# Kernel optimization log

Measured on AMD Instinct MI355X. Metric: run time of the kernel, lower is better.

## Reference

```python
import jax, jax.numpy as jnp
import numpy as np

D = 1024
BATCH = 32768
QJL_DIM = 1024

# Optimal 3-bit (8-level) Lloyd-Max quantizer for the standard normal N(0,1).
# Rotated coordinates of Gaussian inputs are ~N(0,1) since Pi is orthogonal.
_CENTROIDS = np.array([-2.1520, -1.3439, -0.7560, -0.2451,
                        0.2451,  0.7560,  1.3439,  2.1520], dtype=np.float32)
_BOUNDARIES = np.array([-1.7480, -1.0500, -0.5006, 0.0,
                         0.5006,  1.0500,  1.7480], dtype=np.float32)


def setup_inputs() -> dict:
    key = jax.random.key(0)
    kx, kpi, ks = jax.random.split(key, 3)
    x = jax.random.normal(kx, (BATCH, D), dtype=jnp.float32)
    # Haar rotation: orthogonal matrix via QR of a Gaussian matrix
    G = jax.random.normal(kpi, (D, D), dtype=jnp.float32)
    Pi, _ = jnp.linalg.qr(G)
    # QJL projection matrix: iid N(0,1), shape (m, d)
    S = jax.random.normal(ks, (QJL_DIM, D), dtype=jnp.float32)
    return {
        "x": x,
        "Pi": Pi,
        "S": S,
        "centroids": jnp.asarray(_CENTROIDS),
        "boundaries": jnp.asarray(_BOUNDARIES),
    }


def reference(x, Pi, S, centroids, boundaries):
    # --- Stage 1: MSE quantizer (rotate -> Lloyd-Max -> unrotate) ---
    y = x @ Pi.T                                  # (B, d) rotated coordinates
    idx = jnp.searchsorted(boundaries, y)         # (B, d) int32 in [0, 8)
    y_hat = centroids[idx]                        # (B, d) per-coordinate dequant
    x_hat = y_hat @ Pi                            # unrotate back to original frame

    # --- Stage 2: QJL on the residual ---
    residual = x - x_hat                          # (B, d)
    residual_norm = jnp.linalg.norm(residual, axis=-1)   # (B,)
    projected = residual @ S.T                    # (B, m)
    # torch.sign with sign(0) forced to +1
    qjl_signs = jnp.where(projected >= 0, 1.0, -1.0).astype(x.dtype)

    return (idx, qjl_signs, residual_norm)
```

## Files before the change

### kernel.cpp

```cpp
#include <hip/hip_runtime.h>

#define DK 1024
#define NB 32768
#define BM 128
#define BN 128
#define BKT 16

#define MASK_MAIN 0x0000000080000000ull

template<int MODE>
__global__ __launch_bounds__(256)
void gk(const float* __restrict__ A,
        const float* __restrict__ W,
        const float* __restrict__ X,
        const float* __restrict__ cent,
        const float* __restrict__ bnd,
        float* __restrict__ out)
{
    __shared__ float As[BKT][BM];
    __shared__ float Bs[BKT][BN];
    __shared__ float centS[8];

    const int tid = threadIdx.x;
    const int tx8 = tid & 15, ty8 = tid >> 4;
    const int m0 = blockIdx.y * BM;
    const int n0 = blockIdx.x * BN;

    const int arow = tid >> 1;
    const int ak0  = (tid & 1) * 8;
    const int brow = tid >> 4;
    const int bn0  = (tid & 15) * 8;

    if (MODE == 1 && tid < 8) centS[tid] = cent[tid];

    float chn[8][8], tot[8][8];
#pragma unroll
    for (int i = 0; i < 8; ++i)
#pragma unroll
        for (int j = 0; j < 8; ++j) { chn[i][j] = 0.0f; tot[i][j] = 0.0f; }

    for (int kt = 0; kt < DK / BKT; ++kt) {
        const int k0 = kt * BKT;
        __syncthreads();

        {
            const float4 v0 = *(const float4*)&A[(size_t)(m0 + arow) * DK + k0 + ak0];
            const float4 v1 = *(const float4*)&A[(size_t)(m0 + arow) * DK + k0 + ak0 + 4];
            if (MODE == 1) {
                As[ak0 + 0][arow] = centS[(int)v0.x];
                As[ak0 + 1][arow] = centS[(int)v0.y];
                As[ak0 + 2][arow] = centS[(int)v0.z];
                As[ak0 + 3][arow] = centS[(int)v0.w];
                As[ak0 + 4][arow] = centS[(int)v1.x];
                As[ak0 + 5][arow] = centS[(int)v1.y];
                As[ak0 + 6][arow] = centS[(int)v1.z];
                As[ak0 + 7][arow] = centS[(int)v1.w];
            } else {
                As[ak0 + 0][arow] = v0.x;
                As[ak0 + 1][arow] = v0.y;
                As[ak0 + 2][arow] = v0.z;
                As[ak0 + 3][arow] = v0.w;
                As[ak0 + 4][arow] = v1.x;
                As[ak0 + 5][arow] = v1.y;
                As[ak0 + 6][arow] = v1.z;
                As[ak0 + 7][arow] = v1.w;
            }
        }

        if (MODE == 1) {
            const float4 w0 = *(const float4*)&W[(size_t)(k0 + brow) * DK + n0 + bn0];
            const float4 w1 = *(const float4*)&W[(size_t)(k0 + brow) * DK + n0 + bn0 + 4];
            *(float4*)&Bs[brow][bn0]     = w0;
            *(float4*)&Bs[brow][bn0 + 4] = w1;
        } else {
            const float4 w0 = *(const float4*)&W[(size_t)(n0 + arow) * DK + k0 + ak0];
            const float4 w1 = *(const float4*)&W[(size_t)(n0 + arow) * DK + k0 + ak0 + 4];
            Bs[ak0 + 0][arow] = w0.x;
            Bs[ak0 + 1][arow] = w0.y;
            Bs[ak0 + 2][arow] = w0.z;
            Bs[ak0 + 3][arow] = w0.w;
            Bs[ak0 + 4][arow] = w1.x;
            Bs[ak0 + 5][arow] = w1.y;
            Bs[ak0 + 6][arow] = w1.z;
            Bs[ak0 + 7][arow] = w1.w;
        }
        __syncthreads();

#pragma unroll
        for (int kk = 0; kk < BKT; ++kk) {
            float a[8], b[8];
            *(float4*)&a[0] = *(const float4*)&As[kk][ty8 * 8];
            *(float4*)&a[4] = *(const float4*)&As[kk][ty8 * 8 + 4];
            *(float4*)&b[0] = *(const float4*)&Bs[kk][tx8 * 8];
            *(float4*)&b[4] = *(const float4*)&Bs[kk][tx8 * 8 + 4];
#pragma unroll
            for (int i = 0; i < 8; ++i)
#pragma unroll
                for (int j = 0; j < 8; ++j)
                    chn[i][j] = fmaf(a[i], b[j], chn[i][j]);
        }

        if ((MASK_MAIN >> kt) & 1ull) {
#pragma unroll
            for (int i = 0; i < 8; ++i)
#pragma unroll
                for (int j = 0; j < 8; ++j) { tot[i][j] += chn[i][j]; chn[i][j] = 0.0f; }
        }
    }
#pragma unroll
    for (int i = 0; i < 8; ++i)
#pragma unroll
        for (int j = 0; j < 8; ++j) tot[i][j] += chn[i][j];

    if constexpr (MODE == 0) {
        float bb[7];
#pragma unroll
        for (int t = 0; t < 7; ++t) bb[t] = bnd[t];
#pragma unroll
        for (int i = 0; i < 8; ++i)
#pragma unroll
            for (int j = 0; j < 8; ++j) {
                const int row = m0 + ty8 * 8 + i;
                const int col = n0 + tx8 * 8 + j;
                const float yf = tot[i][j];
                int id = 0;
#pragma unroll
                for (int t = 0; t < 7; ++t) id += (yf > bb[t]) ? 1 : 0;
                out[(size_t)row * DK + col] = (float)id;
            }
    } else if constexpr (MODE == 1) {
#pragma unroll
        for (int i = 0; i < 8; ++i)
#pragma unroll
            for (int j = 0; j < 8; ++j) {
                const int row = m0 + ty8 * 8 + i;
                const int col = n0 + tx8 * 8 + j;
                out[(size_t)row * DK + col] = X[(size_t)row * DK + col] - tot[i][j];
            }
    } else {
#pragma unroll
        for (int i = 0; i < 8; ++i)
#pragma unroll
            for (int j = 0; j < 8; ++j) {
                const int row = m0 + ty8 * 8 + i;
                const int col = n0 + tx8 * 8 + j;
                out[(size_t)row * DK + col] = (tot[i][j] >= 0.0f) ? 1.0f : -1.0f;
            }
    }
}

__global__ __launch_bounds__(256)
void norm_k(const float* __restrict__ resid, float* __restrict__ outn)
{
    const int lane = threadIdx.x & 63;
    const int row  = blockIdx.x * 4 + (threadIdx.x >> 6);
    const float* r = &resid[(size_t)row * DK];
    double s = 0.0;
    for (int i = lane; i < DK; i += 64) {
        const double v = (double)r[i];
        s += v * v;
    }
#pragma unroll
    for (int off = 32; off > 0; off >>= 1)
        s += __shfl_xor(s, off, 64);
    if (lane == 0) outn[row] = (float)sqrt(s);
}

__global__ __launch_bounds__(256)
void stage2_band(const float* __restrict__ RS,
                 const float* __restrict__ Sm,
                 float* __restrict__ out_sign,
                 float* __restrict__ out_norm)
{
    __shared__ float Rs[16][DK + 1];
    __shared__ float Bsh[BKT][64];

    const int tid = threadIdx.x;
    const int m0  = blockIdx.x * 16;

    for (int c = tid; c < 16 * 256; c += 256) {
        const int row = c >> 8, q = c & 255;
        const float4 v = *(const float4*)&RS[(size_t)(m0 + row) * DK + q * 4];
        Rs[row][q * 4 + 0] = v.x;
        Rs[row][q * 4 + 1] = v.y;
        Rs[row][q * 4 + 2] = v.z;
        Rs[row][q * 4 + 3] = v.w;
    }
    __syncthreads();

    {
        const int row = tid >> 4, sub = tid & 15;
        double s = 0.0;
        for (int c = sub; c < DK; c += 16) {
            const double v = (double)Rs[row][c];
            s += v * v;
        }
        s += __shfl_xor(s, 1, 16);
        s += __shfl_xor(s, 2, 16);
        s += __shfl_xor(s, 4, 16);
        s += __shfl_xor(s, 8, 16);
        if (sub == 0) out_norm[m0 + row] = (float)sqrt(s);
    }

    const int tx = tid & 15, ty = tid >> 4;
    const int srow = tid >> 2, s4 = tid & 3;

    for (int nt = 0; nt < 16; ++nt) {
        const int n0 = nt * 64;
        float chn[4] = {0.f, 0.f, 0.f, 0.f}, tot[4] = {0.f, 0.f, 0.f, 0.f};

        for (int kt = 0; kt < DK / BKT; ++kt) {
            const int k0 = kt * BKT;
            __syncthreads();
            const float4 w = *(const float4*)&Sm[(size_t)(n0 + srow) * DK + k0 + s4 * 4];
            Bsh[s4 * 4 + 0][srow] = w.x;
            Bsh[s4 * 4 + 1][srow] = w.y;
            Bsh[s4 * 4 + 2][srow] = w.z;
            Bsh[s4 * 4 + 3][srow] = w.w;
            __syncthreads();
#pragma unroll
            for (int kk = 0; kk < BKT; ++kk) {
                const float a = Rs[ty][k0 + kk];
#pragma unroll
                for (int j = 0; j < 4; ++j)
                    chn[j] = fmaf(a, Bsh[kk][tx * 4 + j], chn[j]);
            }
            if ((MASK_MAIN >> kt) & 1ull) {
#pragma unroll
                for (int j = 0; j < 4; ++j) { tot[j] += chn[j]; chn[j] = 0.0f; }
            }
        }
#pragma unroll
        for (int j = 0; j < 4; ++j) tot[j] += chn[j];
#pragma unroll
        for (int j = 0; j < 4; ++j)
            out_sign[(size_t)(m0 + ty) * DK + n0 + tx * 4 + j] =
                (tot[j] >= 0.0f) ? 1.0f : -1.0f;
    }
}

extern "C" void kernel_launch(void* const* d_in, const int* in_sizes, int n_in,
                              void* d_out, int out_size, void* d_ws, size_t ws_size,
                              hipStream_t stream)
{
    const float* x    = (const float*)d_in[0];
    const float* Pi   = (const float*)d_in[1];
    const float* S    = (const float*)d_in[2];
    const float* cent = (const float*)d_in[3];
    const float* bnd  = (const float*)d_in[4];

    float* out_idx  = (float*)d_out;
    float* out_sign = out_idx + (size_t)NB * DK;
    float* out_norm = out_idx + 2 * (size_t)NB * DK;

    const dim3 grid(DK / BN, NB / BM);
    const size_t needF32 = (size_t)NB * DK * sizeof(float);

    gk<0><<<grid, 256, 0, stream>>>(x, Pi, (const float*)nullptr, cent, bnd, out_idx);

    if (ws_size >= needF32) {
        float* resid = (float*)d_ws;
        gk<1><<<grid, 256, 0, stream>>>(out_idx, Pi, x, cent, bnd, resid);
        gk<2><<<grid, 256, 0, stream>>>(resid, S, (const float*)nullptr, cent, bnd, out_sign);
        norm_k<<<NB / 4, 256, 0, stream>>>(resid, out_norm);
    } else {
        gk<1><<<grid, 256, 0, stream>>>(out_idx, Pi, x, cent, bnd, out_sign);
        stage2_band<<<NB / 16, 256, 0, stream>>>(out_sign, S, out_sign, out_norm);
    }
}
```

Before: 3.758 ms.

## Prefetch next K-tile into registers, pad LDS, vectorize epilogue stores

The generic GEMM kernel now loads the next K tile from global memory into registers while computing on the current tile, doubling the K tile size to 32. LDS arrays are padded with a row stride of 144 and a group offset to reduce bank conflicts. Epilogue stores and X reads are vectorized to float4. The accumulation split point is preserved, so numerics match the previous scheme. The cost is more registers for the prefetch buffers and more LDS per block, which may lower occupancy.

Result: faster. 3.463 ms (-7.8%).

```diff
diff --git a/kernel.cpp b/kernel.cpp
--- a/kernel.cpp
+++ b/kernel.cpp
@@ -4,9 +4,12 @@
 #define NB 32768
 #define BM 128
 #define BN 128
-#define BKT 16
-
-#define MASK_MAIN 0x0000000080000000ull
+#define BKT 32
+#define NKT (DK / BKT)
+#define FLUSH_KT 15
+#define RSF 144
+
+__device__ __forceinline__ int gcol(int c) { return c + ((c >> 5) << 2); }
 
 template<int MODE>
 __global__ __launch_bounds__(256)
@@ -17,8 +20,8 @@
         const float* __restrict__ bnd,
         float* __restrict__ out)
 {
-    __shared__ float As[BKT][BM];
-    __shared__ float Bs[BKT][BN];
+    __shared__ float As[BKT * RSF];
+    __shared__ float Bs[BKT * RSF];
     __shared__ float centS[8];
 
     const int tid = threadIdx.x;
@@ -26,73 +29,82 @@
     const int m0 = blockIdx.y * BM;
     const int n0 = blockIdx.x * BN;
 
-    const int arow = tid >> 1;
-    const int ak0  = (tid & 1) * 8;
-    const int brow = tid >> 4;
-    const int bn0  = (tid & 15) * 8;
+    const int arow  = tid >> 1;
+    const int ak0   = (tid & 1) * 16;
+    const int arowG = arow + ((arow >> 5) << 2);
+    const int brow = tid >> 3;
+    const int bn0  = (tid & 7) * 16;
 
     if (MODE == 1 && tid < 8) centS[tid] = cent[tid];
 
+    const int aoff = ty8 * 8 + ((ty8 >> 2) << 2);
+    const int boff = tx8 * 8 + ((tx8 >> 2) << 2);
+
+    float4 pa[4], pb[4];
+
+    auto load_tile = [&](int kt) {
+        const int k0 = kt * BKT;
+        const float* ap = &A[(size_t)(m0 + arow) * DK + k0 + ak0];
+        pa[0] = *(const float4*)(ap + 0);
+        pa[1] = *(const float4*)(ap + 4);
+        pa[2] = *(const float4*)(ap + 8);
+        pa[3] = *(const float4*)(ap + 12);
+        if (MODE == 1) {
+            const float* bp = &W[(size_t)(k0 + brow) * DK + n0 + bn0];
+            pb[0] = *(const float4*)(bp + 0);
+            pb[1] = *(const float4*)(bp + 4);
+            pb[2] = *(const float4*)(bp + 8);
+            pb[3] = *(const float4*)(bp + 12);
+        } else {
+            const float* bp = &W[(size_t)(n0 + arow) * DK + k0 + ak0];
+            pb[0] = *(const float4*)(bp + 0);
+            pb[1] = *(const float4*)(bp + 4);
+            pb[2] = *(const float4*)(bp + 8);
+            pb[3] = *(const float4*)(bp + 12);
+        }
+    };
+
+    auto write_lds = [&]() {
+        const float* pf = (const float*)pa;
+        if (MODE == 1) {
+#pragma unroll
+            for (int e = 0; e < 16; ++e)
+                As[(ak0 + e) * RSF + arowG] = centS[(int)pf[e]];
+#pragma unroll
+            for (int q = 0; q < 4; ++q)
+                *(float4*)&Bs[brow * RSF + gcol(bn0 + q * 4)] = pb[q];
+        } else {
+#pragma unroll
+            for (int e = 0; e < 16; ++e)
+                As[(ak0 + e) * RSF + arowG] = pf[e];
+            const float* qf = (const float*)pb;
+#pragma unroll
+            for (int e = 0; e < 16; ++e)
+                Bs[(ak0 + e) * RSF + arowG] = qf[e];
+        }
+    };
+
     float chn[8][8], tot[8][8];
 #pragma unroll
     for (int i = 0; i < 8; ++i)
 #pragma unroll
         for (int j = 0; j < 8; ++j) { chn[i][j] = 0.0f; tot[i][j] = 0.0f; }
 
-    for (int kt = 0; kt < DK / BKT; ++kt) {
-        const int k0 = kt * BKT;
-        __syncthreads();
-
-        {
-            const float4 v0 = *(const float4*)&A[(size_t)(m0 + arow) * DK + k0 + ak0];
-            const float4 v1 = *(const float4*)&A[(size_t)(m0 + arow) * DK + k0 + ak0 + 4];
-            if (MODE == 1) {
-                As[ak0 + 0][arow] = centS[(int)v0.x];
-                As[ak0 + 1][arow] = centS[(int)v0.y];
-                As[ak0 + 2][arow] = centS[(int)v0.z];
-                As[ak0 + 3][arow] = centS[(int)v0.w];
-                As[ak0 + 4][arow] = centS[(int)v1.x];
-                As[ak0 + 5][arow] = centS[(int)v1.y];
-                As[ak0 + 6][arow] = centS[(int)v1.z];
-                As[ak0 + 7][arow] = centS[(int)v1.w];
-            } else {
-                As[ak0 + 0][arow] = v0.x;
-                As[ak0 + 1][arow] = v0.y;
-                As[ak0 + 2][arow] = v0.z;
-                As[ak0 + 3][arow] = v0.w;
-                As[ak0 + 4][arow] = v1.x;
-                As[ak0 + 5][arow] = v1.y;
-                As[ak0 + 6][arow] = v1.z;
-                As[ak0 + 7][arow] = v1.w;
-            }
-        }
-
-        if (MODE == 1) {
-            const float4 w0 = *(const float4*)&W[(size_t)(k0 + brow) * DK + n0 + bn0];
-            const float4 w1 = *(const float4*)&W[(size_t)(k0 + brow) * DK + n0 + bn0 + 4];
-            *(float4*)&Bs[brow][bn0]     = w0;
-            *(float4*)&Bs[brow][bn0 + 4] = w1;
-        } else {
-            const float4 w0 = *(const float4*)&W[(size_t)(n0 + arow) * DK + k0 + ak0];
-            const float4 w1 = *(const float4*)&W[(size_t)(n0 + arow) * DK + k0 + ak0 + 4];
-            Bs[ak0 + 0][arow] = w0.x;
-            Bs[ak0 + 1][arow] = w0.y;
-            Bs[ak0 + 2][arow] = w0.z;
-            Bs[ak0 + 3][arow] = w0.w;
-            Bs[ak0 + 4][arow] = w1.x;
-            Bs[ak0 + 5][arow] = w1.y;
-            Bs[ak0 + 6][arow] = w1.z;
-            Bs[ak0 + 7][arow] = w1.w;
-        }
+    load_tile(0);
+    __syncthreads();
+    write_lds();
+
+    for (int kt = 0; kt < NKT; ++kt) {
+        if (kt + 1 < NKT) load_tile(kt + 1);
         __syncthreads();
 
 #pragma unroll
         for (int kk = 0; kk < BKT; ++kk) {
             float a[8], b[8];
-            *(float4*)&a[0] = *(const float4*)&As[kk][ty8 * 8];
-            *(float4*)&a[4] = *(const float4*)&As[kk][ty8 * 8 + 4];
-            *(float4*)&b[0] = *(const float4*)&Bs[kk][tx8 * 8];
-            *(float4*)&b[4] = *(const float4*)&Bs[kk][tx8 * 8 + 4];
+            *(float4*)&a[0] = *(const float4*)&As[kk * RSF + aoff];
+            *(float4*)&a[4] = *(const float4*)&As[kk * RSF + aoff + 4];
+            *(float4*)&b[0] = *(const float4*)&Bs[kk * RSF + boff];
+            *(float4*)&b[4] = *(const float4*)&Bs[kk * RSF + boff + 4];
 #pragma unroll
             for (int i = 0; i < 8; ++i)
 #pragma unroll
@@ -100,12 +112,15 @@
                     chn[i][j] = fmaf(a[i], b[j], chn[i][j]);
         }
 
-        if ((MASK_MAIN >> kt) & 1ull) {
+        if (kt == FLUSH_KT) {
 #pragma unroll
             for (int i = 0; i < 8; ++i)
 #pragma unroll
                 for (int j = 0; j < 8; ++j) { tot[i][j] += chn[i][j]; chn[i][j] = 0.0f; }
         }
+
+        __syncthreads();
+        if (kt + 1 < NKT) write_lds();
     }
 #pragma unroll
     for (int i = 0; i < 8; ++i)
@@ -117,35 +132,51 @@
 #pragma unroll
         for (int t = 0; t < 7; ++t) bb[t] = bnd[t];
 #pragma unroll
-        for (int i = 0; i < 8; ++i)
-#pragma unroll
-            for (int j = 0; j < 8; ++j) {
-                const int row = m0 + ty8 * 8 + i;
-                const int col = n0 + tx8 * 8 + j;
-                const float yf = tot[i][j];
-                int id = 0;
-#pragma unroll
-                for (int t = 0; t < 7; ++t) id += (yf > bb[t]) ? 1 : 0;
-                out[(size_t)row * DK + col] = (float)id;
-            }
+        for (int i = 0; i < 8; ++i) {
+            const int row = m0 + ty8 * 8 + i;
+#pragma unroll
+            for (int jq = 0; jq < 2; ++jq) {
+                float4 v;
+#pragma unroll
+                for (int e = 0; e < 4; ++e) {
+                    const float yf = tot[i][jq * 4 + e];
+                    int id = 0;
+#pragma unroll
+                    for (int t = 0; t < 7; ++t) id += (yf > bb[t]) ? 1 : 0;
+                    ((float*)&v)[e] = (float)id;
+                }
+                *(float4*)&out[(size_t)row * DK + n0 + tx8 * 8 + jq * 4] = v;
+            }
+        }
     } else if constexpr (MODE == 1) {
 #pragma unroll
-        for (int i = 0; i < 8; ++i)
-#pragma unroll
-            for (int j = 0; j < 8; ++j) {
-                const int row = m0 + ty8 * 8 + i;
-                const int col = n0 + tx8 * 8 + j;
-                out[(size_t)row * DK + col] = X[(size_t)row * DK + col] - tot[i][j];
-            }
+        for (int i = 0; i < 8; ++i) {
+            const int row = m0 + ty8 * 8 + i;
+#pragma unroll
+            for (int jq = 0; jq < 2; ++jq) {
+                const int col = n0 + tx8 * 8 + jq * 4;
+                const float4 xv = *(const float4*)&X[(size_t)row * DK + col];
+                float4 v;
+                v.x = xv.x - tot[i][jq * 4 + 0];
+                v.y = xv.y - tot[i][jq * 4 + 1];
+                v.z = xv.z - tot[i][jq * 4 + 2];
+                v.w = xv.w - tot[i][jq * 4 + 3];
+                *(float4*)&out[(size_t)row * DK + col] = v;
+            }
+        }
     } else {
 #pragma unroll
-        for (int i = 0; i < 8; ++i)
-#pragma unroll
-            for (int j = 0; j < 8; ++j) {
-                const int row = m0 + ty8 * 8 + i;
-                const int col = n0 + tx8 * 8 + j;
-                out[(size_t)row * DK + col] = (tot[i][j] >= 0.0f) ? 1.0f : -1.0f;
-            }
+        for (int i = 0; i < 8; ++i) {
+            const int row = m0 + ty8 * 8 + i;
+#pragma unroll
+            for (int jq = 0; jq < 2; ++jq) {
+                float4 v;
+#pragma unroll
+                for (int e = 0; e < 4; ++e)
+                    ((float*)&v)[e] = (tot[i][jq * 4 + e] >= 0.0f) ? 1.0f : -1.0f;
+                *(float4*)&out[(size_t)row * DK + n0 + tx8 * 8 + jq * 4] = v;
+            }
+        }
     }
 }
 
@@ -173,7 +204,7 @@
                  float* __restrict__ out_norm)
 {
     __shared__ float Rs[16][DK + 1];
-    __shared__ float Bsh[BKT][64];
+    __shared__ float Bsh[16][64];
 
     const int tid = threadIdx.x;
     const int m0  = blockIdx.x * 16;
@@ -209,8 +240,8 @@
         const int n0 = nt * 64;
         float chn[4] = {0.f, 0.f, 0.f, 0.f}, tot[4] = {0.f, 0.f, 0.f, 0.f};
 
-        for (int kt = 0; kt < DK / BKT; ++kt) {
-            const int k0 = kt * BKT;
+        for (int kt = 0; kt < 64; ++kt) {
+            const int k0 = kt * 16;
             __syncthreads();
             const float4 w = *(const float4*)&Sm[(size_t)(n0 + srow) * DK + k0 + s4 * 4];
             Bsh[s4 * 4 + 0][srow] = w.x;
@@ -219,13 +250,13 @@
             Bsh[s4 * 4 + 3][srow] = w.w;
             __syncthreads();
 #pragma unroll
-            for (int kk = 0; kk < BKT; ++kk) {
+            for (int kk = 0; kk < 16; ++kk) {
                 const float a = Rs[ty][k0 + kk];
 #pragma unroll
                 for (int j = 0; j < 4; ++j)
                     chn[j] = fmaf(a, Bsh[kk][tx * 4 + j], chn[j]);
             }
-            if ((MASK_MAIN >> kt) & 1ull) {
+            if (kt == 31) {
 #pragma unroll
                 for (int j = 0; j < 4; ++j) { tot[j] += chn[j]; chn[j] = 0.0f; }
             }
```
